# Kernel optimization log

Hardware: AMD Instinct MI355X
Metric: run time of the kernel (lower is better)

Reference implementation:

```python
import jax, jax.numpy as jnp
import numpy as np

B, S, N = 1, 512, 256
C_M, C_Z, C_OPM, C_H, H = 64, 128, 32, 32, 8
INF = 1.0e6


def layer_norm(x, w, b, eps=1e-5):
    mu = x.mean(-1, keepdims=True)
    var = x.var(-1, keepdims=True)
    return (x - mu) / jnp.sqrt(var + eps) * w + b


def setup_inputs() -> dict:
    key = jax.random.key(0)
    ks = jax.random.split(key, 12)
    inp = {
        'm': jax.random.normal(ks[0], (B, S, N, C_M), jnp.float32),
        'z': jax.random.normal(ks[1], (B, N, N, C_Z), jnp.float32),
        'msa_mask': jnp.ones((B, S, N), jnp.float32),
        'pair_mask': jnp.ones((B, N, N), jnp.float32),
        # OuterProductMean params
        'opm_norm_w': jnp.ones((C_M,), jnp.float32),
        'opm_norm_b': jnp.zeros((C_M,), jnp.float32),
        'opm_a_w': jax.random.normal(ks[2], (C_OPM, C_M), jnp.float32) * 0.05,
        'opm_b_w': jax.random.normal(ks[3], (C_OPM, C_M), jnp.float32) * 0.05,
        'opm_o_w': jax.random.normal(ks[4], (C_Z, C_OPM * C_OPM), jnp.float32) * 0.02,
        'opm_o_b': jnp.zeros((C_Z,), jnp.float32),
        # PairWeightedAveraging params
        'pwa_norm_m_w': jnp.ones((C_M,), jnp.float32),
        'pwa_norm_m_b': jnp.zeros((C_M,), jnp.float32),
        'pwa_norm_z_w': jnp.ones((C_Z,), jnp.float32),
        'pwa_norm_z_b': jnp.zeros((C_Z,), jnp.float32),
        'pwa_m_w': jax.random.normal(ks[5], (H * C_H, C_M), jnp.float32) * 0.05,
        'pwa_g_w': jax.random.normal(ks[6], (H * C_H, C_M), jnp.float32) * 0.05,
        'pwa_z_w': jax.random.normal(ks[7], (H, C_Z), jnp.float32) * 0.05,
        'pwa_o_w': jax.random.normal(ks[8], (C_M, H * C_H), jnp.float32) * 0.02,
    }
    return inp


def reference(m, z, msa_mask, pair_mask,
              opm_norm_w, opm_norm_b, opm_a_w, opm_b_w, opm_o_w, opm_o_b,
              pwa_norm_m_w, pwa_norm_m_b, pwa_norm_z_w, pwa_norm_z_b,
              pwa_m_w, pwa_g_w, pwa_z_w, pwa_o_w):
    # ---- OuterProductMean: m (B,S,N,c_in), msa_mask (B,S,N) -> (B,N,N,c_z)
    mn = layer_norm(m, opm_norm_w, opm_norm_b)
    a = jnp.einsum('bsni,ci->bsnc', mn, opm_a_w) * msa_mask[..., None]  # (B,S,N,c)
    bb = jnp.einsum('bsni,ci->bsnc', mn, opm_b_w) * msa_mask[..., None]
    num_mask = jnp.clip(jnp.einsum('bsi,bsj->bij', msa_mask, msa_mask), 1.0)
    # outer product mean over S; flatten (c,d) with c-major to match torch reshape
    zt = jnp.einsum('bsic,bsjd->bijcd', a, bb).reshape(B, N, N, C_OPM * C_OPM)
    zt = zt / num_mask[..., None]
    z_opm = zt @ opm_o_w.T + opm_o_b  # (B,N,N,c_z)
    z_new = z + z_opm

    # ---- PairWeightedAveraging: m (B,S,N,c_m), z_new (B,N,N,c_z) -> (B,S,N,c_m)
    mn2 = layer_norm(m, pwa_norm_m_w, pwa_norm_m_b)
    zn = layer_norm(z_new, pwa_norm_z_w, pwa_norm_z_b)
    v = (mn2 @ pwa_m_w.T).reshape(B, S, N, H, C_H)            # (B,S,N,H,ch)
    bias = jnp.einsum('bijz,hz->bhij', zn, pwa_z_w)            # (B,H,N,N)
    bias = bias + (1.0 - pair_mask[:, None]) * (-INF)
    w = jax.nn.softmax(bias, axis=-1)
    g = jax.nn.sigmoid(mn2 @ pwa_g_w.T)                        # (B,S,N,H*ch)
    o = jnp.einsum('bhij,bsjhc->bsihc', w, v).reshape(B, S, N, H * C_H)
    out = (g * o) @ pwa_o_w.T                                  # (B,S,N,c_m)
    return out
```

## Files before the change

kernel.cpp:

```cpp
#include <hip/hip_runtime.h>
#include <stdint.h>

using u16 = unsigned short;
using u32 = unsigned int;

#define S_DIM 512
#define N_DIM 256
#define CM 64
#define CZ 128
#define NH 8
#define NPOS (S_DIM*N_DIM)
#define NPAIR (N_DIM*N_DIM)
#define CHS 256
#define CHPOS (CHS*N_DIM)

__device__ __forceinline__ float b2f(u16 h){ u32 u = ((u32)h)<<16; float f; __builtin_memcpy(&f,&u,4); return f; }
__device__ __forceinline__ u16 f2b(float f){ u32 u; __builtin_memcpy(&u,&f,4); u32 r = (u + 0x7fffu + ((u>>16)&1u))>>16; return (u16)r; }

typedef __bf16 bf16_t;
typedef bf16_t bf16x8 __attribute__((ext_vector_type(8)));
typedef float  f32x4  __attribute__((ext_vector_type(4)));

typedef const __attribute__((address_space(1))) void* gvp;
typedef __attribute__((address_space(3))) void* lvp;
#define GLOAD_LDS16(g, l) __builtin_amdgcn_global_load_lds((gvp)(uintptr_t)(g), (lvp)(uintptr_t)(l), 16, 0, 0)

__device__ __forceinline__ uint4 bfmul8(uint4 a, uint4 b){
  union{uint4 v; u16 h[8];} x,y,r;
  x.v=a; y.v=b;
  #pragma unroll
  for (int k=0;k<8;k++) r.h[k] = f2b(b2f(x.h[k])*b2f(y.h[k]));
  return r.v;
}

struct EpiArgs {
  const float* rowscale;
  u16*  out_b;
  float* out_f;
  int ldc;
};

constexpr int EPI_PLAIN=0, EPI_ROWSCALE=1, EPI_SIGMOID=2, EPI_VT=3, EPI_O=6;

template<int BM,int BN,int WR,int WC,int FM,int FN,int EPI,bool MULA=false>
__global__ __launch_bounds__(256) void gemm_k(const u16* __restrict__ A, const u16* __restrict__ A2,
                                              const u16* __restrict__ W,
                                              int K, size_t sAz, size_t sWz, EpiArgs ea)
{
  static_assert(BM==WR*FM*16 && BN==WC*FN*16 && WR*WC==4, "geom");
  __shared__ __align__(16) u16 ls[(BM+BN)*64];
  u16* lsA = ls;
  u16* lsW = ls + BM*64;
  const int tid  = threadIdx.x;
  const int lane = tid & 63;
  const int wv   = tid >> 6;
  const int wr   = wv / WC;
  const int wc   = wv % WC;
  const int m0   = blockIdx.y * BM;
  const int n0   = blockIdx.x * BN;
  const u16* Ab  = A  + (size_t)blockIdx.z * sAz + (size_t)m0 * K;
  const u16* A2b = MULA ? (A2 + (size_t)blockIdx.z * sAz + (size_t)m0 * K) : nullptr;
  const u16* Wb  = W  + (size_t)blockIdx.z * sWz + (size_t)n0 * K;

  f32x4 acc[FM][FN];
  #pragma unroll
  for (int i=0;i<FM;i++)
    #pragma unroll
    for (int j=0;j<FN;j++) acc[i][j] = (f32x4){0.f,0.f,0.f,0.f};

  const int nkt = K >> 6;
  for (int kt = 0; kt < nkt; ++kt) {
    if constexpr (!MULA) {
      #pragma unroll
      for (int c0 = 0; c0 < BM*8; c0 += 256) {
        int cc = c0 + (wv<<6) + lane;
        int row = cc>>3, kc = cc&7;
        GLOAD_LDS16(Ab + (size_t)row*K + (kt<<6) + ((kc ^ (row&7))<<3),
                    lsA + (size_t)(c0 + (wv<<6))*8);
      }
      #pragma unroll
      for (int c0 = 0; c0 < BN*8; c0 += 256) {
        int cc = c0 + (wv<<6) + lane;
        int row = cc>>3, kc = cc&7;
        GLOAD_LDS16(Wb + (size_t)row*K + (kt<<6) + ((kc ^ (row&7))<<3),
                    lsW + (size_t)(c0 + (wv<<6))*8);
      }
    } else {
      for (int c = tid; c < (BM+BN)*8; c += 256) {
        if (c < BM*8) {
          int row = c>>3, kc = c&7;
          size_t off = (size_t)row*K + (kt<<6) + (kc<<3);
          uint4 v = *reinterpret_cast<const uint4*>(Ab + off);
          uint4 v2 = *reinterpret_cast<const uint4*>(A2b + off);
          v = bfmul8(v, v2);
          *reinterpret_cast<uint4*>((char*)lsA + row*128 + ((kc<<4) ^ ((row&7)<<4))) = v;
        } else {
          int c2 = c - BM*8; int row = c2>>3, kc = c2&7;
          uint4 v = *reinterpret_cast<const uint4*>(Wb + (size_t)row*K + (kt<<6) + (kc<<3));
          *reinterpret_cast<uint4*>((char*)lsW + row*128 + ((kc<<4) ^ ((row&7)<<4))) = v;
        }
      }
    }
    __syncthreads();
    #pragma unroll
    for (int kk=0; kk<2; ++kk) {
      const int kb = (kk<<6) + ((lane>>4)<<4);
      bf16x8 af[FM], wf[FN];
      #pragma unroll
      for (int mf=0;mf<FM;mf++){
        int row = wr*FM*16 + mf*16 + (lane&15);
        af[mf] = *reinterpret_cast<const bf16x8*>((char*)lsA + row*128 + (kb ^ ((row&7)<<4)));
      }
      #pragma unroll
      for (int nf=0;nf<FN;nf++){
        int row = wc*FN*16 + nf*16 + (lane&15);
        wf[nf] = *reinterpret_cast<const bf16x8*>((char*)lsW + row*128 + (kb ^ ((row&7)<<4)));
      }
      #pragma unroll
      for (int mf=0;mf<FM;mf++)
        #pragma unroll
        for (int nf=0;nf<FN;nf++)
          acc[mf][nf] = __builtin_amdgcn_mfma_f32_16x16x32_bf16(af[mf], wf[nf], acc[mf][nf], 0,0,0);
    }
    __syncthreads();
  }

  if constexpr (EPI==EPI_VT) {
    #pragma unroll
    for (int mf=0;mf<FM;mf++){
      #pragma unroll
      for (int nf=0;nf<FN;nf++){
        f32x4 v = acc[mf][nf];
        int hcrow = wc*FN*16 + nf*16 + (lane&15);
        int jl0   = wr*FM*16 + mf*16 + ((lane>>4)<<2);
        union { uint2 u; u16 h[4]; } pk;
        #pragma unroll
        for (int r=0;r<4;r++) pk.h[r] = f2b(v[r]);
        *reinterpret_cast<uint2*>((char*)ls + hcrow*256 + ((jl0*2) ^ ((hcrow&7)<<4))) = pk.u;
      }
    }
    __syncthreads();
    const int sl = m0>>8, j0 = m0&255, hb = n0>>5;
    #pragma unroll
    for (int itc=0; itc<8; ++itc){
      int idx = itc*256 + tid;
      int hcrow = idx>>4, q = idx&15;
      uint4 vv = *reinterpret_cast<const uint4*>((char*)ls + hcrow*256 + ((q*16) ^ ((hcrow&7)<<4)));
      int dstrow = (hb + (hcrow>>5))*(CHS*32) + sl*32 + (hcrow&31);
      *reinterpret_cast<uint4*>(ea.out_b + (size_t)dstrow*N_DIM + j0 + q*8) = vv;
    }
  } else {
    const int hz = blockIdx.z;
    #pragma unroll
    for (int mf=0;mf<FM;mf++){
      #pragma unroll
      for (int nf=0;nf<FN;nf++){
        f32x4 v = acc[mf][nf];
        int col   = n0 + wc*FN*16 + nf*16 + (lane&15);
        int rbase = m0 + wr*FM*16 + mf*16 + ((lane>>4)<<2);
        #pragma unroll
        for (int r=0;r<4;r++){
          int row = rbase + r;
          float x = v[r];
          if constexpr (EPI==EPI_PLAIN) {
            ea.out_f[(size_t)row*ea.ldc + col] = x;
          } else if constexpr (EPI==EPI_ROWSCALE) {
            x *= ea.rowscale[row];
            ea.out_b[(size_t)row*ea.ldc + col] = f2b(x);
          } else if constexpr (EPI==EPI_SIGMOID) {
            x = 1.f/(1.f+__expf(-x));
            ea.out_b[(size_t)row*ea.ldc + col] = f2b(x);
          } else if constexpr (EPI==EPI_O) {
            int sl2 = col>>5, cc = col&31;
            ea.out_b[(size_t)(sl2*N_DIM + row)*256 + hz*32 + cc] = f2b(x);
          }
        }
      }
    }
  }
}

__global__ __launch_bounds__(256,1) void opm_fused(const u16* __restrict__ a_t, const u16* __restrict__ b_t,
                                                   const float* __restrict__ recip, const u16* __restrict__ owp,
                                                   const float* __restrict__ obias, const float* __restrict__ z,
                                                   float* __restrict__ z_new)
{
  __shared__ __align__(16) u16 ls[24576];
  const int tid = threadIdx.x, lane = tid&63, wv = tid>>6;
  const int wr = wv>>1, wc = wv&1;
  const int bid = blockIdx.x;
  const int xcd = bid&7, l = bid>>3;
  const int by = ((xcd>>1)<<4) + (l&15);
  const int bx = ((xcd&1)<<5) + (l>>4);
  const u16* Ab = a_t + (size_t)by*128*S_DIM;
  const u16* Wb = b_t + (size_t)bx*128*S_DIM;
  u16* lsA = ls;
  u16* lsW = ls + 8192;

  f32x4 acc[4][4];
  #pragma unroll
  for (int i=0;i<4;i++)
    #pragma unroll
    for (int j=0;j<4;j++) acc[i][j] = (f32x4){0.f,0.f,0.f,0.f};

  for (int kt = 0; kt < 8; ++kt) {
    #pragma unroll
    for (int c0 = 0; c0 < 1024; c0 += 256) {
      int cc = c0 + (wv<<6) + lane;
      int row = cc>>3, kc = cc&7;
      size_t srcoff = (size_t)row*S_DIM + (kt<<6) + ((kc ^ (row&7))<<3);
      GLOAD_LDS16(Ab + srcoff, lsA + (size_t)(c0 + (wv<<6))*8);
      GLOAD_LDS16(Wb + srcoff, lsW + (size_t)(c0 + (wv<<6))*8);
    }
    __syncthreads();
    #pragma unroll
    for (int kk=0; kk<2; ++kk) {
      const int kb = (kk<<6) + ((lane>>4)<<4);
      bf16x8 af[4], wf[4];
      #pragma unroll
      for (int mf=0;mf<4;mf++){
        int row = wr*64 + mf*16 + (lane&15);
        af[mf] = *reinterpret_cast<const bf16x8*>((char*)lsA + row*128 + (kb ^ ((row&7)<<4)));
      }
      #pragma unroll
      for (int nf=0;nf<4;nf++){
        int row = wc*64 + nf*16 + (lane&15);
        wf[nf] = *reinterpret_cast<const bf16x8*>((char*)lsW + row*128 + (kb ^ ((row&7)<<4)));
      }
      #pragma unroll
      for (int mf=0;mf<4;mf++)
        #pragma unroll
        for (int nf=0;nf<4;nf++)
          acc[mf][nf] = __builtin_amdgcn_mfma_f32_16x16x32_bf16(af[mf], wf[nf], acc[mf][nf], 0,0,0);
    }
    __syncthreads();
  }

  #pragma unroll
  for (int mf=0;mf<4;mf++){
    #pragma unroll
    for (int nf=0;nf<4;nf++){
      int ii = 2*wr + (mf>>1);
      int jj = 2*wc + (nf>>1);
      int p  = ii*4 + jj;
      int d  = ((nf&1)<<4) + (lane&15);
      int c0 = ((mf&1)<<4) + ((lane>>4)<<2);
      float rv = recip[(by*4+ii)*N_DIM + bx*4 + jj];
      f32x4 v = acc[mf][nf];
      union { uint2 u; u16 h[4]; } pk;
      #pragma unroll
      for (int r=0;r<4;r++) pk.h[r] = f2b(v[r]*rv);
      int byte = p*2048 + (((d + p)&31)<<6) + ((c0*2) ^ (((d>>1)&3)<<4));
      *reinterpret_cast<uint2*>((char*)ls + byte) = pk.u;
    }
  }
  __syncthreads();

  f32x4 acc2[2] = {(f32x4){0,0,0,0},(f32x4){0,0,0,0}};
  u16* lsw2 = ls + 16384 + wv*2048;
  const u16* owpw = owp + wv*2048;
  for (int it=0; it<16; ++it){
    #pragma unroll
    for (int j=0;j<4;j++)
      GLOAD_LDS16(owpw + (size_t)it*8192 + j*512 + lane*8, lsw2 + j*512);
    asm volatile("s_waitcnt vmcnt(0)" ::: "memory");
    __builtin_amdgcn_sched_barrier(0);
    #pragma unroll
    for (int kk=0; kk<2; ++kk){
      int d = it*2 + kk;
      int p  = lane&15;
      int c0 = (lane>>4)<<3;
      bf16x8 af = *reinterpret_cast<const bf16x8*>((char*)ls + p*2048 + (((d + p)&31)<<6) +
                    ((c0*2) ^ (((d>>1)&3)<<4)));
      const int kb = (kk<<6) + ((lane>>4)<<4);
      #pragma unroll
      for (int nf=0;nf<2;nf++){
        int rl = nf*16 + (lane&15);
        bf16x8 wf = *reinterpret_cast<const bf16x8*>((char*)lsw2 + rl*128 + (kb ^ ((rl&7)<<4)));
        acc2[nf] = __builtin_amdgcn_mfma_f32_16x16x32_bf16(af, wf, acc2[nf], 0,0,0);
      }
    }
    __builtin_amdgcn_sched_barrier(0);
  }

  #pragma unroll
  for (int nf=0;nf<2;nf++){
    int col = wv*32 + nf*16 + (lane&15);
    #pragma unroll
    for (int r=0;r<4;r++){
      int p = ((lane>>4)<<2) + r;
      size_t gp = (size_t)(by*4 + (p>>2))*N_DIM + bx*4 + (p&3);
      z_new[gp*CZ + col] = acc2[nf][r] + obias[col] + z[gp*CZ + col];
    }
  }
}

__global__ __launch_bounds__(256) void ln_m_kernel(const float* __restrict__ m, const float* ow, const float* ob,
                                                   const float* pw, const float* pb,
                                                   u16* __restrict__ mo, u16* __restrict__ mp)
{
  int row  = blockIdx.x*4 + (threadIdx.x>>6);
  int lane = threadIdx.x & 63;
  float x = m[(size_t)row*CM + lane];
  float s = x, s2 = x*x;
  #pragma unroll
  for (int off=32; off; off>>=1){ s += __shfl_xor(s,off); s2 += __shfl_xor(s2,off); }
  float mu   = s*(1.f/64.f);
  float var  = s2*(1.f/64.f) - mu*mu;
  float rstd = rsqrtf(var + 1e-5f);
  float mn = (x-mu)*rstd;
  mo[(size_t)row*CM+lane] = f2b(mn*ow[lane] + ob[lane]);
  mp[(size_t)row*CM+lane] = f2b(mn*pw[lane] + pb[lane]);
}

__global__ __launch_bounds__(256) void cvt_w_kernel(const float* __restrict__ aw, const float* __restrict__ bw,
                                                    const float* __restrict__ ow, const float* __restrict__ mw,
                                                    const float* __restrict__ gw, const float* __restrict__ o2w,
                                                    u16* __restrict__ wb)
{
  int e = blockIdx.x*256 + threadIdx.x;
  float v;
  if (e < 4096)        { int r = e>>6, c = e&63; v = (r<32)? aw[r*64+c] : bw[(r-32)*64+c]; }
  else if (e < 135168) { int t = e-4096; int it = t>>13, rem = t&8191, row = rem>>6, h = rem&63;
                         int kl = h ^ ((row&7)<<3);
                         int kp = it*64 + kl;
                         int d = kp>>5, c = kp&31;
                         v = ow[row*1024 + c*32 + d]; }
  else if (e < 151552) { v = mw[e-135168]; }
  else if (e < 167936) { v = gw[e-151552]; }
  else                 { v = o2w[e-167936]; }
  wb[e] = f2b(v);
}

__global__ __launch_bounds__(256) void transpose_ab_kernel(const u16* __restrict__ ab,
                                                           u16* __restrict__ a_t, u16* __restrict__ b_t)
{
  __shared__ u16 t[64][72];
  int sb = blockIdx.x, i = blockIdx.y, tid = threadIdx.x;
  for (int c = tid; c < 512; c += 256){
    int sl = c>>3, kc = c&7;
    union { uint4 v; u16 h[8]; } u;
    u.v = *reinterpret_cast<const uint4*>(ab + ((size_t)(sb*64+sl)*N_DIM + i)*64 + (kc<<3));
    #pragma unroll
    for (int k=0;k<8;k++) t[sl][kc*8+k] = u.h[k];
  }
  __syncthreads();
  for (int c = tid; c < 512; c += 256){
    int cc = c>>3, sc = c&7;
    union { uint4 v; u16 h[8]; } u;
    #pragma unroll
    for (int k=0;k<8;k++) u.h[k] = t[sc*8+k][cc];
    u16* dst = (cc < 32) ? (a_t + (size_t)(i*32+cc)*S_DIM) : (b_t + (size_t)(i*32+cc-32)*S_DIM);
    *reinterpret_cast<uint4*>(dst + sb*64 + (sc<<3)) = u.v;
  }
}

__global__ __launch_bounds__(256) void num_mask_kernel(const float* __restrict__ msa, float* __restrict__ recip){
  int i = blockIdx.x, j = threadIdx.x;
  float s = 0.f;
  #pragma unroll 8
  for (int t=0;t<S_DIM;t++) s += msa[t*N_DIM+i] * msa[t*N_DIM+j];
  recip[i*N_DIM + j] = 1.f / fmaxf(s, 1.f);
}

__global__ __launch_bounds__(256) void ln_bias_kernel(const float* __restrict__ z_new, const float* zw, const float* zb,
                                                      const float* zwh, const float* pm, float* __restrict__ bias)
{
  int p    = blockIdx.x*4 + (threadIdx.x>>6);
  int lane = threadIdx.x & 63;
  const float* zr = z_new + (size_t)p*CZ;
  float x0 = zr[lane*2], x1 = zr[lane*2+1];
  float s = x0+x1, s2 = x0*x0 + x1*x1;
  #pragma unroll
  for (int off=32; off; off>>=1){ s += __shfl_xor(s,off); s2 += __shfl_xor(s2,off); }
  float mu   = s*(1.f/128.f);
  float var  = s2*(1.f/128.f) - mu*mu;
  float rstd = rsqrtf(var + 1e-5f);
  float zn0 = (x0-mu)*rstd*zw[lane*2]   + zb[lane*2];
  float zn1 = (x1-mu)*rstd*zw[lane*2+1] + zb[lane*2+1];
  float bm = (1.f - pm[p]) * (-1.0e6f);
  float outv = 0.f;
  #pragma unroll
  for (int hh=0; hh<8; hh++){
    float tp = zn0*zwh[hh*CZ + lane*2] + zn1*zwh[hh*CZ + lane*2+1];
    #pragma unroll
    for (int off=32; off; off>>=1) tp += __shfl_xor(tp,off);
    if (lane == hh) outv = tp + bm;
  }
  if (lane < 8) bias[(size_t)lane*NPAIR + p] = outv;
}

__global__ __launch_bounds__(256) void softmax_kernel(const float* __restrict__ bias, u16* __restrict__ w_sm){
  int r    = blockIdx.x*4 + (threadIdx.x>>6);
  int lane = threadIdx.x & 63;
  const float* src = bias + (size_t)(r>>8)*NPAIR + (size_t)(r&255)*N_DIM;
  float4 xv = *reinterpret_cast<const float4*>(src + lane*4);
  float mx = fmaxf(fmaxf(xv.x,xv.y), fmaxf(xv.z,xv.w));
  #pragma unroll
  for (int off=32; off; off>>=1) mx = fmaxf(mx, __shfl_xor(mx,off));
  float e0 = __expf(xv.x-mx), e1 = __expf(xv.y-mx), e2 = __expf(xv.z-mx), e3 = __expf(xv.w-mx);
  float s = e0+e1+e2+e3;
  #pragma unroll
  for (int off=32; off; off>>=1) s += __shfl_xor(s,off);
  float rs = 1.f/s;
  ushort4 st; st.x=f2b(e0*rs); st.y=f2b(e1*rs); st.z=f2b(e2*rs); st.w=f2b(e3*rs);
  *reinterpret_cast<ushort4*>(w_sm + (size_t)r*N_DIM + lane*4) = st;
}

extern "C" void kernel_launch(void* const* d_in, const int* in_sizes, int n_in,
                              void* d_out, int out_size, void* d_ws, size_t ws_size,
                              hipStream_t stream)
{
  const float* m      = (const float*)d_in[0];
  const float* z      = (const float*)d_in[1];
  const float* msa    = (const float*)d_in[2];
  const float* pmask  = (const float*)d_in[3];
  const float* opm_nw = (const float*)d_in[4];
  const float* opm_nb = (const float*)d_in[5];
  const float* opm_aw = (const float*)d_in[6];
  const float* opm_bw = (const float*)d_in[7];
  const float* opm_ow = (const float*)d_in[8];
  const float* opm_ob = (const float*)d_in[9];
  const float* pwa_nmw= (const float*)d_in[10];
  const float* pwa_nmb= (const float*)d_in[11];
  const float* pwa_nzw= (const float*)d_in[12];
  const float* pwa_nzb= (const float*)d_in[13];
  const float* pwa_mw = (const float*)d_in[14];
  const float* pwa_gw = (const float*)d_in[15];
  const float* pwa_zw = (const float*)d_in[16];
  const float* pwa_ow = (const float*)d_in[17];
  float* out = (float*)d_out;
  char* ws = (char*)d_ws;

  const size_t MB = 1024*1024;
  u16*  mn_pwa = (u16*)(ws + 0);
  u16*  mn_opm = (u16*)(ws + 16*MB);
  u16*  ab     = (u16*)(ws + 32*MB);
  u16*  a_t    = (u16*)(ws + 48*MB);
  u16*  b_t    = (u16*)(ws + 56*MB);
  float* z_new = (float*)(ws + 64*MB);
  float* bias  = (float*)(ws + 128*MB);
  u16*  w_sm   = (u16*)(ws + 130*MB);
  float* recip = (float*)(ws + 131*MB);
  u16*  wb     = (u16*)(ws + 131*MB + 512*1024);
  u16*  v_t  = (u16*)(ws + 16*MB);
  u16*  gbuf = (u16*)(ws + 48*MB);
  u16*  obuf = (u16*)(ws + 80*MB);

  const u16* w_ab = wb;
  const u16* owp  = wb + 4096;
  const u16* mw_b = wb + 135168;
  const u16* gw_b = wb + 151552;
  const u16* ow_b = wb + 167936;

  ln_m_kernel<<<dim3(NPOS/4),256,0,stream>>>(m, opm_nw, opm_nb, pwa_nmw, pwa_nmb, mn_opm, mn_pwa);
  cvt_w_kernel<<<dim3(184320/256),256,0,stream>>>(opm_aw, opm_bw, opm_ow, pwa_mw, pwa_gw, pwa_ow, wb);
  { EpiArgs ea{}; ea.rowscale = msa; ea.out_b = ab; ea.ldc = 64;
    gemm_k<128,64,2,2,4,2,EPI_ROWSCALE><<<dim3(1,NPOS/128),256,0,stream>>>(mn_opm, nullptr, w_ab, 64, 0,0, ea); }
  transpose_ab_kernel<<<dim3(8,256),256,0,stream>>>(ab, a_t, b_t);
  num_mask_kernel<<<dim3(256),256,0,stream>>>(msa, recip);
  opm_fused<<<dim3(4096),256,0,stream>>>(a_t, b_t, recip, owp, opm_ob, z, z_new);
  ln_bias_kernel<<<dim3(NPAIR/4),256,0,stream>>>(z_new, pwa_nzw, pwa_nzb, pwa_zw, pmask, bias);
  softmax_kernel<<<dim3(2048/4),256,0,stream>>>(bias, w_sm);

  for (int sc=0; sc<2; ++sc){
    const u16* mnp = mn_pwa + (size_t)sc*CHPOS*CM;
    { EpiArgs ea{}; ea.out_b = v_t;
      gemm_k<128,128,2,2,4,4,EPI_VT><<<dim3(2,CHPOS/128),256,0,stream>>>(mnp, nullptr, mw_b, 64, 0,0, ea); }
    { EpiArgs ea{}; ea.out_b = gbuf; ea.ldc = 256;
      gemm_k<128,128,2,2,4,4,EPI_SIGMOID><<<dim3(2,CHPOS/128),256,0,stream>>>(mnp, nullptr, gw_b, 64, 0,0, ea); }
    { EpiArgs ea{}; ea.out_b = obuf;
      gemm_k<128,128,2,2,4,4,EPI_O><<<dim3((CHS*32)/128, 2, NH),256,0,stream>>>(w_sm, nullptr, v_t, 256,
            (size_t)NPAIR, (size_t)(CHS*32)*N_DIM, ea); }
    { EpiArgs ea{}; ea.out_f = out + (size_t)sc*CHPOS*CM; ea.ldc = 64;
      gemm_k<128,64,2,2,4,2,EPI_PLAIN,true><<<dim3(1,CHPOS/128),256,0,stream>>>(gbuf, obuf, ow_b, 256, 0,0, ea); }
  }
}
```

Before: 523.5 us.

## Double-buffer LDS loads in fused outer-product-mean kernel; bake constant GEMM args

The fused OPM kernel grows its LDS to 64KB and double-buffers both stages. The next K-tile of a/b, or the next chunk of the output weights, is fetched with async global-to-LDS loads while MFMAs run on the current buffer, using partial vmcnt waits and raw s_barriers. The generic GEMM kernel becomes a device body wrapped in per-use kernels with K and strides fixed at compile time. The larger LDS footprint can lower occupancy, though the kernel already declares one block per CU, and the hand-placed waits depend on exact load-count accounting.

New measurement: 495.1 us. -5.4%, faster.

```diff
diff --git a/kernel.cpp b/kernel.cpp
--- a/kernel.cpp
+++ b/kernel.cpp
@@ -42,10 +42,10 @@
 
 constexpr int EPI_PLAIN=0, EPI_ROWSCALE=1, EPI_SIGMOID=2, EPI_VT=3, EPI_O=6;
 
-template<int BM,int BN,int WR,int WC,int FM,int FN,int EPI,bool MULA=false>
-__global__ __launch_bounds__(256) void gemm_k(const u16* __restrict__ A, const u16* __restrict__ A2,
-                                              const u16* __restrict__ W,
-                                              int K, size_t sAz, size_t sWz, EpiArgs ea)
+template<int BM,int BN,int WR,int WC,int FM,int FN,int EPI,bool MULA>
+__device__ __forceinline__ void gemm_body(const u16* __restrict__ A, const u16* __restrict__ A2,
+                                          const u16* __restrict__ W,
+                                          int K, size_t sAz, size_t sWz, EpiArgs ea)
 {
   static_assert(BM==WR*FM*16 && BN==WC*FN*16 && WR*WC==4, "geom");
   __shared__ __align__(16) u16 ls[(BM+BN)*64];
@@ -180,12 +180,28 @@
   }
 }
 
+__global__ __launch_bounds__(256) void k_rowscale(const u16* A, const u16* W, EpiArgs ea){
+  gemm_body<128,64,2,2,4,2,EPI_ROWSCALE,false>(A,nullptr,W,64,0,0,ea);
+}
+__global__ __launch_bounds__(256) void k_vt(const u16* A, const u16* W, EpiArgs ea){
+  gemm_body<128,128,2,2,4,4,EPI_VT,false>(A,nullptr,W,64,0,0,ea);
+}
+__global__ __launch_bounds__(256) void k_sig(const u16* A, const u16* W, EpiArgs ea){
+  gemm_body<128,128,2,2,4,4,EPI_SIGMOID,false>(A,nullptr,W,64,0,0,ea);
+}
+__global__ __launch_bounds__(256) void k_o(const u16* A, const u16* W, EpiArgs ea){
+  gemm_body<128,128,2,2,4,4,EPI_O,false>(A,nullptr,W,256,(size_t)NPAIR,(size_t)(CHS*32)*N_DIM,ea);
+}
+__global__ __launch_bounds__(256) void k_go(const u16* A, const u16* A2, const u16* W, EpiArgs ea){
+  gemm_body<128,64,2,2,4,2,EPI_PLAIN,true>(A,A2,W,256,0,0,ea);
+}
+
 __global__ __launch_bounds__(256,1) void opm_fused(const u16* __restrict__ a_t, const u16* __restrict__ b_t,
                                                    const float* __restrict__ recip, const u16* __restrict__ owp,
                                                    const float* __restrict__ obias, const float* __restrict__ z,
                                                    float* __restrict__ z_new)
 {
-  __shared__ __align__(16) u16 ls[24576];
+  __shared__ __align__(16) u16 ls[32768];
   const int tid = threadIdx.x, lane = tid&63, wv = tid>>6;
   const int wr = wv>>1, wc = wv&1;
   const int bid = blockIdx.x;
@@ -194,8 +210,8 @@
   const int bx = ((xcd&1)<<5) + (l>>4);
   const u16* Ab = a_t + (size_t)by*128*S_DIM;
   const u16* Wb = b_t + (size_t)bx*128*S_DIM;
-  u16* lsA = ls;
-  u16* lsW = ls + 8192;
+  u16* buf0 = ls;
+  u16* buf1 = ls + 16384;
 
   f32x4 acc[4][4];
   #pragma unroll
@@ -203,16 +219,32 @@
     #pragma unroll
     for (int j=0;j<4;j++) acc[i][j] = (f32x4){0.f,0.f,0.f,0.f};
 
-  for (int kt = 0; kt < 8; ++kt) {
+  auto stage1 = [&](u16* b, int kt){
     #pragma unroll
     for (int c0 = 0; c0 < 1024; c0 += 256) {
       int cc = c0 + (wv<<6) + lane;
       int row = cc>>3, kc = cc&7;
       size_t srcoff = (size_t)row*S_DIM + (kt<<6) + ((kc ^ (row&7))<<3);
-      GLOAD_LDS16(Ab + srcoff, lsA + (size_t)(c0 + (wv<<6))*8);
-      GLOAD_LDS16(Wb + srcoff, lsW + (size_t)(c0 + (wv<<6))*8);
-    }
-    __syncthreads();
+      GLOAD_LDS16(Ab + srcoff, b + (size_t)(c0 + (wv<<6))*8);
+      GLOAD_LDS16(Wb + srcoff, b + 8192 + (size_t)(c0 + (wv<<6))*8);
+    }
+  };
+
+  stage1(buf0, 0);
+  for (int kt = 0; kt < 8; ++kt) {
+    u16* cur = (kt&1) ? buf1 : buf0;
+    u16* nxt = (kt&1) ? buf0 : buf1;
+    if (kt < 7) {
+      stage1(nxt, kt+1);
+      asm volatile("s_waitcnt vmcnt(8)" ::: "memory");
+    } else {
+      asm volatile("s_waitcnt vmcnt(0)" ::: "memory");
+    }
+    __builtin_amdgcn_sched_barrier(0);
+    __builtin_amdgcn_s_barrier();
+    __builtin_amdgcn_sched_barrier(0);
+    u16* lsA = cur;
+    u16* lsW = cur + 8192;
     #pragma unroll
     for (int kk=0; kk<2; ++kk) {
       const int kb = (kk<<6) + ((lane>>4)<<4);
@@ -233,8 +265,20 @@
         for (int nf=0;nf<4;nf++)
           acc[mf][nf] = __builtin_amdgcn_mfma_f32_16x16x32_bf16(af[mf], wf[nf], acc[mf][nf], 0,0,0);
     }
-    __syncthreads();
-  }
+    __builtin_amdgcn_sched_barrier(0);
+    __builtin_amdgcn_s_barrier();
+    __builtin_amdgcn_sched_barrier(0);
+  }
+
+  const u16* owpw = owp + wv*2048;
+  auto stage2 = [&](int it){
+    const u16* src = owpw + (size_t)it*8192;
+    u16* dst = buf1 + ((it&1) ? 8192 : 0) + wv*2048;
+    #pragma unroll
+    for (int j=0;j<4;j++)
+      GLOAD_LDS16(src + j*512 + lane*8, dst + j*512);
+  };
+  stage2(0);
 
   #pragma unroll
   for (int mf=0;mf<4;mf++){
@@ -254,17 +298,20 @@
       *reinterpret_cast<uint2*>((char*)ls + byte) = pk.u;
     }
   }
-  __syncthreads();
+  asm volatile("s_waitcnt lgkmcnt(0)" ::: "memory");
+  __builtin_amdgcn_s_barrier();
+  __builtin_amdgcn_sched_barrier(0);
 
   f32x4 acc2[2] = {(f32x4){0,0,0,0},(f32x4){0,0,0,0}};
-  u16* lsw2 = ls + 16384 + wv*2048;
-  const u16* owpw = owp + wv*2048;
   for (int it=0; it<16; ++it){
-    #pragma unroll
-    for (int j=0;j<4;j++)
-      GLOAD_LDS16(owpw + (size_t)it*8192 + j*512 + lane*8, lsw2 + j*512);
-    asm volatile("s_waitcnt vmcnt(0)" ::: "memory");
+    if (it < 15){
+      stage2(it+1);
+      asm volatile("s_waitcnt vmcnt(4)" ::: "memory");
+    } else {
+      asm volatile("s_waitcnt vmcnt(0)" ::: "memory");
+    }
     __builtin_amdgcn_sched_barrier(0);
+    u16* sl2 = buf1 + ((it&1) ? 8192 : 0) + wv*2048;
     #pragma unroll
     for (int kk=0; kk<2; ++kk){
       int d = it*2 + kk;
@@ -276,7 +323,7 @@
       #pragma unroll
       for (int nf=0;nf<2;nf++){
         int rl = nf*16 + (lane&15);
-        bf16x8 wf = *reinterpret_cast<const bf16x8*>((char*)lsw2 + rl*128 + (kb ^ ((rl&7)<<4)));
+        bf16x8 wf = *reinterpret_cast<const bf16x8*>((char*)sl2 + rl*128 + (kb ^ ((rl&7)<<4)));
         acc2[nf] = __builtin_amdgcn_mfma_f32_16x16x32_bf16(af, wf, acc2[nf], 0,0,0);
       }
     }
@@ -456,7 +503,7 @@
   ln_m_kernel<<<dim3(NPOS/4),256,0,stream>>>(m, opm_nw, opm_nb, pwa_nmw, pwa_nmb, mn_opm, mn_pwa);
   cvt_w_kernel<<<dim3(184320/256),256,0,stream>>>(opm_aw, opm_bw, opm_ow, pwa_mw, pwa_gw, pwa_ow, wb);
   { EpiArgs ea{}; ea.rowscale = msa; ea.out_b = ab; ea.ldc = 64;
-    gemm_k<128,64,2,2,4,2,EPI_ROWSCALE><<<dim3(1,NPOS/128),256,0,stream>>>(mn_opm, nullptr, w_ab, 64, 0,0, ea); }
+    k_rowscale<<<dim3(1,NPOS/128),256,0,stream>>>(mn_opm, w_ab, ea); }
   transpose_ab_kernel<<<dim3(8,256),256,0,stream>>>(ab, a_t, b_t);
   num_mask_kernel<<<dim3(256),256,0,stream>>>(msa, recip);
   opm_fused<<<dim3(4096),256,0,stream>>>(a_t, b_t, recip, owp, opm_ob, z, z_new);
@@ -466,13 +513,12 @@
   for (int sc=0; sc<2; ++sc){
     const u16* mnp = mn_pwa + (size_t)sc*CHPOS*CM;
     { EpiArgs ea{}; ea.out_b = v_t;
-      gemm_k<128,128,2,2,4,4,EPI_VT><<<dim3(2,CHPOS/128),256,0,stream>>>(mnp, nullptr, mw_b, 64, 0,0, ea); }
+      k_vt<<<dim3(2,CHPOS/128),256,0,stream>>>(mnp, mw_b, ea); }
     { EpiArgs ea{}; ea.out_b = gbuf; ea.ldc = 256;
-      gemm_k<128,128,2,2,4,4,EPI_SIGMOID><<<dim3(2,CHPOS/128),256,0,stream>>>(mnp, nullptr, gw_b, 64, 0,0, ea); }
+      k_sig<<<dim3(2,CHPOS/128),256,0,stream>>>(mnp, gw_b, ea); }
     { EpiArgs ea{}; ea.out_b = obuf;
-      gemm_k<128,128,2,2,4,4,EPI_O><<<dim3((CHS*32)/128, 2, NH),256,0,stream>>>(w_sm, nullptr, v_t, 256,
-            (size_t)NPAIR, (size_t)(CHS*32)*N_DIM, ea); }
+      k_o<<<dim3((CHS*32)/128, 2, NH),256,0,stream>>>(w_sm, v_t, ea); }
     { EpiArgs ea{}; ea.out_f = out + (size_t)sc*CHPOS*CM; ea.ldc = 64;
-      gemm_k<128,64,2,2,4,2,EPI_PLAIN,true><<<dim3(1,CHPOS/128),256,0,stream>>>(gbuf, obuf, ow_b, 256, 0,0, ea); }
-  }
-}
+      k_go<<<dim3(1,CHPOS/128),256,0,stream>>>(gbuf, obuf, ow_b, ea); }
+  }
+}
```
